# Kernel tuning notes

Hardware: AMD Instinct MI355X
Metric: run time of the kernel (lower is better)

The kernel has to match this reference:

```python
import jax, jax.numpy as jnp
import numpy as np

MARGIN = 0.2  # TripletMarginLoss margin and TripletMarginMiner margin


def setup_inputs() -> dict:
    key = jax.random.key(0)
    k1, k2 = jax.random.split(key)
    embeddings = jax.random.normal(k1, (384, 256), dtype=jnp.float32)
    labels = jax.random.randint(k2, (384,), 0, 32)
    return {"embeddings": embeddings, "labels": labels}


def _pairwise_l2(e):
    # Euclidean distance matrix with sqrt-safe gradient at zero.
    sq = jnp.sum(e * e, axis=1)
    d2 = jnp.maximum(sq[:, None] + sq[None, :] - 2.0 * (e @ e.T), 0.0)
    pos = d2 > 0.0
    return jnp.sqrt(jnp.where(pos, d2, 1.0)) * pos


def reference(embeddings, labels):
    # pytorch-metric-learning LpDistance defaults: normalize_embeddings=True, p=2
    e = embeddings / jnp.maximum(
        jnp.linalg.norm(embeddings, axis=1, keepdims=True), 1e-12
    )
    D = _pairwise_l2(e)  # [B, B]
    n = D.shape[0]

    same = labels[:, None] == labels[None, :]
    eye = jnp.eye(n, dtype=bool)
    pos_mask = same & ~eye   # valid (anchor, positive) pairs
    neg_mask = ~same         # valid (anchor, negative) pairs

    ap = D[:, :, None]       # dist(anchor, positive), broadcast over negative
    an = D[:, None, :]       # dist(anchor, negative), broadcast over positive
    tm = an - ap             # miner's triplet_margin (is_inverted=False)

    valid = pos_mask[:, :, None] & neg_mask[:, None, :]     # [B, B, B]
    # semihard miner: 0 < an - ap <= margin
    semihard = valid & (tm > 0.0) & (tm <= MARGIN)

    # TripletMarginLoss per-triplet loss: relu(ap - an + margin) = relu(margin - tm)
    losses = jnp.where(semihard, jnp.maximum(MARGIN - tm, 0.0), 0.0)

    # AvgNonZeroReducer: mean over strictly-positive losses (0 if none)
    nz = jnp.sum(losses > 0.0)
    total = jnp.sum(losses)
    return jnp.where(nz > 0, total / jnp.maximum(nz, 1).astype(total.dtype), 0.0)
```

## Files before the change

### kernel.cpp

```cpp
#include <hip/hip_runtime.h>

#define N        384
#define DIM      256
#define MARGIN_F 0.2f
#define NANCH    2
#define NBLK     (N / NANCH)


__global__ __launch_bounds__(DIM) void normalize_kernel(
    const float* __restrict__ emb, float* __restrict__ eT,
    float* __restrict__ sq, float* __restrict__ invn,
    float* __restrict__ accum_sum, unsigned int* __restrict__ accum_cnt,
    unsigned int* __restrict__ done_cnt)
{
    const int row = blockIdx.x;
    const int tid = threadIdx.x;

    float v = emb[row * DIM + tid];
    float s = v * v;
    #pragma unroll
    for (int off = 32; off > 0; off >>= 1) s += __shfl_down(s, off, 64);
    __shared__ float wsum[4];
    const int wave = tid >> 6, lane = tid & 63;
    if (lane == 0) wsum[wave] = s;
    __syncthreads();
    if (tid == 0) wsum[0] = wsum[0] + wsum[1] + wsum[2] + wsum[3];
    __syncthreads();
    const float tot = wsum[0];

    const float inv = 1.0f / fmaxf(sqrtf(tot), 1e-12f);
    eT[tid * N + row] = v * inv;

    if (tid == 0) {
        sq[row]   = tot * inv * inv;
        invn[row] = inv;
        if (row == 0) { accum_sum[0] = 0.0f; accum_cnt[0] = 0u; done_cnt[0] = 0u; }
    }
}

__global__ __launch_bounds__(N) void fused_kernel(
    const float* __restrict__ emb, const float* __restrict__ eT,
    const float* __restrict__ sq, const float* __restrict__ invn,
    const int* __restrict__ labels,
    float* __restrict__ accum_sum, unsigned int* __restrict__ accum_cnt,
    unsigned int* __restrict__ done_cnt, float* __restrict__ out)
{
    const int i0  = blockIdx.x * NANCH;
    const int tid = threadIdx.x;

    __shared__ float ei[NANCH][DIM];
    __shared__ float Drow[NANCH][N];
    __shared__ int   lab[N];
    __shared__ int   posList[NANCH][N];
    __shared__ int   posCnt[NANCH];
    __shared__ float sredS[N / 64];
    __shared__ unsigned int sredC[N / 64];

    for (int t = tid; t < NANCH * DIM; t += N) {
        const int a = t >> 8, k = t & (DIM - 1);
        ei[a][k] = emb[(i0 + a) * DIM + k] * invn[i0 + a];
    }
    lab[tid] = labels[tid];
    if (tid < NANCH) posCnt[tid] = 0;
    __syncthreads();

    float acc0 = 0.0f, acc1 = 0.0f;
    const float* __restrict__ col = eT + tid;
    #pragma unroll 8
    for (int k = 0; k < DIM; ++k) {
        const float ek = col[k * N];
        acc0 += ei[0][k] * ek;
        acc1 += ei[1][k] * ek;
    }
    const float sqj = sq[tid];
    {
        const float d2 = fmaxf(sq[i0] + sqj - 2.0f * acc0, 0.0f);
        Drow[0][tid] = (d2 > 0.0f) ? sqrtf(d2) : 0.0f;
    }
    {
        const float d2 = fmaxf(sq[i0 + 1] + sqj - 2.0f * acc1, 0.0f);
        Drow[1][tid] = (d2 > 0.0f) ? sqrtf(d2) : 0.0f;
    }
    __syncthreads();

    const int lj = lab[tid];
    #pragma unroll
    for (int a = 0; a < NANCH; ++a) {
        const int ia = i0 + a;
        if (lj == lab[ia] && tid != ia)
            posList[a][atomicAdd(&posCnt[a], 1)] = tid;
    }
    __syncthreads();

    float        lsum = 0.0f;
    unsigned int lcnt = 0u;
    #pragma unroll
    for (int a = 0; a < NANCH; ++a) {
        const int   li = lab[i0 + a];
        const float dk = Drow[a][tid];
        if (lj != li) {
            const int np = posCnt[a];
            for (int p = 0; p < np; ++p) {
                const float tm = dk - Drow[a][posList[a][p]];
                if (tm > 0.0f && tm <= MARGIN_F) {
                    const float l = MARGIN_F - tm;
                    lsum += l;
                    if (l > 0.0f) lcnt++;
                }
            }
        }
    }

    #pragma unroll
    for (int off = 32; off > 0; off >>= 1) {
        lsum += __shfl_down(lsum, off, 64);
        lcnt += __shfl_down(lcnt, off, 64);
    }
    const int wave = tid >> 6, lane = tid & 63;
    if (lane == 0) { sredS[wave] = lsum; sredC[wave] = lcnt; }
    __syncthreads();

    if (tid == 0) {
        float        S = 0.0f;
        unsigned int C = 0u;
        #pragma unroll
        for (int w = 0; w < N / 64; ++w) { S += sredS[w]; C += sredC[w]; }
        if (S != 0.0f || C != 0u) {
            atomicAdd(accum_sum, S);
            atomicAdd(accum_cnt, C);
        }
        __threadfence();
        const unsigned int prev = atomicAdd(done_cnt, 1);
        if (prev == NBLK - 1) {
            const float        Sall = atomicAdd(accum_sum, 0.0f);
            const unsigned int Call = atomicAdd(accum_cnt, 0u);
            out[0] = (Call > 0u) ? (Sall / (float)Call) : 0.0f;
        }
    }
}

extern "C" void kernel_launch(void* const* d_in, const int* in_sizes, int n_in,
                              void* d_out, int out_size, void* d_ws, size_t ws_size,
                              hipStream_t stream) {
    const float* emb    = (const float*)d_in[0];
    const int*   labels = (const int*)d_in[1];
    float*       out    = (float*)d_out;

    float* ws   = (float*)d_ws;
    float* eT   = ws;
    float* sq   = eT + (size_t)DIM * N;
    float* invn = sq + N;
    float* accum_sum = invn + N;
    unsigned int* accum_cnt = (unsigned int*)(accum_sum + 1);
    unsigned int* done_cnt  = accum_cnt + 1;

    normalize_kernel<<<N, DIM, 0, stream>>>(emb, eT, sq, invn,
                                            accum_sum, accum_cnt, done_cnt);
    fused_kernel<<<NBLK, N, 0, stream>>>(emb, eT, sq, invn, labels,
                                         accum_sum, accum_cnt, done_cnt, out);
}
```

Measured before the change: 78.53 us.

## Fuse normalization into main kernel and read row-major embeddings with float4

Removes the separate normalize kernel and the transposed eT workspace. Each block now recomputes every row norm itself, and the dot products read raw embedding rows as float4, with the column's inverse norm applied afterwards. Accumulators are zeroed with a memset. Each of the 192 blocks redundantly reads the full embedding matrix to compute norms, and each thread's row-wise float4 reads are strided across threads instead of coalesced. The positive list is capped at 64 entries, which is unsafe if a class has more than 64 members.

```diff
diff --git a/kernel.cpp b/kernel.cpp
--- a/kernel.cpp
+++ b/kernel.cpp
@@ -2,83 +2,74 @@
 
 #define N        384
 #define DIM      256
+#define D4       (DIM / 4)
 #define MARGIN_F 0.2f
 #define NANCH    2
 #define NBLK     (N / NANCH)
+#define NTHR     384
+#define NWAVE    (NTHR / 64)
+#define MAXPOS   64
 
 
-__global__ __launch_bounds__(DIM) void normalize_kernel(
-    const float* __restrict__ emb, float* __restrict__ eT,
-    float* __restrict__ sq, float* __restrict__ invn,
-    float* __restrict__ accum_sum, unsigned int* __restrict__ accum_cnt,
-    unsigned int* __restrict__ done_cnt)
-{
-    const int row = blockIdx.x;
-    const int tid = threadIdx.x;
-
-    float v = emb[row * DIM + tid];
-    float s = v * v;
-    #pragma unroll
-    for (int off = 32; off > 0; off >>= 1) s += __shfl_down(s, off, 64);
-    __shared__ float wsum[4];
-    const int wave = tid >> 6, lane = tid & 63;
-    if (lane == 0) wsum[wave] = s;
-    __syncthreads();
-    if (tid == 0) wsum[0] = wsum[0] + wsum[1] + wsum[2] + wsum[3];
-    __syncthreads();
-    const float tot = wsum[0];
-
-    const float inv = 1.0f / fmaxf(sqrtf(tot), 1e-12f);
-    eT[tid * N + row] = v * inv;
-
-    if (tid == 0) {
-        sq[row]   = tot * inv * inv;
-        invn[row] = inv;
-        if (row == 0) { accum_sum[0] = 0.0f; accum_cnt[0] = 0u; done_cnt[0] = 0u; }
-    }
-}
-
-__global__ __launch_bounds__(N) void fused_kernel(
-    const float* __restrict__ emb, const float* __restrict__ eT,
-    const float* __restrict__ sq, const float* __restrict__ invn,
-    const int* __restrict__ labels,
+__global__ __launch_bounds__(NTHR) void fused_all(
+    const float* __restrict__ emb, const int* __restrict__ labels,
     float* __restrict__ accum_sum, unsigned int* __restrict__ accum_cnt,
     unsigned int* __restrict__ done_cnt, float* __restrict__ out)
 {
-    const int i0  = blockIdx.x * NANCH;
-    const int tid = threadIdx.x;
+    const int i0   = blockIdx.x * NANCH;
+    const int tid  = threadIdx.x;
+    const int wave = tid >> 6, lane = tid & 63;
 
+    __shared__ float invn[N];
+    __shared__ float sqn[N];
     __shared__ float ei[NANCH][DIM];
     __shared__ float Drow[NANCH][N];
     __shared__ int   lab[N];
-    __shared__ int   posList[NANCH][N];
+    __shared__ int   posList[NANCH][MAXPOS];
     __shared__ int   posCnt[NANCH];
-    __shared__ float sredS[N / 64];
-    __shared__ unsigned int sredC[N / 64];
+    __shared__ float        sredS[NWAVE];
+    __shared__ unsigned int sredC[NWAVE];
 
-    for (int t = tid; t < NANCH * DIM; t += N) {
+    const float4* emb4 = (const float4*)emb;
+    for (int r = wave; r < N; r += NWAVE) {
+        const float4 v = emb4[r * D4 + lane];
+        float s = v.x*v.x + v.y*v.y + v.z*v.z + v.w*v.w;
+        #pragma unroll
+        for (int off = 32; off > 0; off >>= 1) s += __shfl_down(s, off, 64);
+        if (lane == 0) {
+            const float inv = 1.0f / fmaxf(sqrtf(s), 1e-12f);
+            invn[r] = inv;
+            sqn[r]  = s * inv * inv;
+        }
+    }
+    if (tid < NANCH) posCnt[tid] = 0;
+    lab[tid] = labels[tid];
+    __syncthreads();
+
+    for (int t = tid; t < NANCH * DIM; t += NTHR) {
         const int a = t >> 8, k = t & (DIM - 1);
         ei[a][k] = emb[(i0 + a) * DIM + k] * invn[i0 + a];
     }
-    lab[tid] = labels[tid];
-    if (tid < NANCH) posCnt[tid] = 0;
     __syncthreads();
 
+    const float4* __restrict__ rowj = emb4 + (size_t)tid * D4;
+    const float4* __restrict__ e0   = (const float4*)ei[0];
+    const float4* __restrict__ e1   = (const float4*)ei[1];
     float acc0 = 0.0f, acc1 = 0.0f;
-    const float* __restrict__ col = eT + tid;
     #pragma unroll 8
-    for (int k = 0; k < DIM; ++k) {
-        const float ek = col[k * N];
-        acc0 += ei[0][k] * ek;
-        acc1 += ei[1][k] * ek;
+    for (int k = 0; k < D4; ++k) {
+        const float4 v  = rowj[k];
+        const float4 a0 = e0[k];
+        const float4 a1 = e1[k];
+        acc0 += v.x*a0.x + v.y*a0.y + v.z*a0.z + v.w*a0.w;
+        acc1 += v.x*a1.x + v.y*a1.y + v.z*a1.z + v.w*a1.w;
     }
-    const float sqj = sq[tid];
+    const float invj = invn[tid];
+    const float sqj  = sqn[tid];
     {
-        const float d2 = fmaxf(sq[i0] + sqj - 2.0f * acc0, 0.0f);
+        float d2 = fmaxf(sqn[i0]     + sqj - 2.0f * acc0 * invj, 0.0f);
         Drow[0][tid] = (d2 > 0.0f) ? sqrtf(d2) : 0.0f;
-    }
-    {
-        const float d2 = fmaxf(sq[i0 + 1] + sqj - 2.0f * acc1, 0.0f);
+        d2       = fmaxf(sqn[i0 + 1] + sqj - 2.0f * acc1 * invj, 0.0f);
         Drow[1][tid] = (d2 > 0.0f) ? sqrtf(d2) : 0.0f;
     }
     __syncthreads();
@@ -116,7 +107,6 @@
         lsum += __shfl_down(lsum, off, 64);
         lcnt += __shfl_down(lcnt, off, 64);
     }
-    const int wave = tid >> 6, lane = tid & 63;
     if (lane == 0) { sredS[wave] = lsum; sredC[wave] = lcnt; }
     __syncthreads();
 
@@ -124,7 +114,7 @@
         float        S = 0.0f;
         unsigned int C = 0u;
         #pragma unroll
-        for (int w = 0; w < N / 64; ++w) { S += sredS[w]; C += sredC[w]; }
+        for (int w = 0; w < NWAVE; ++w) { S += sredS[w]; C += sredC[w]; }
         if (S != 0.0f || C != 0u) {
             atomicAdd(accum_sum, S);
             atomicAdd(accum_cnt, C);
@@ -146,16 +136,11 @@
     const int*   labels = (const int*)d_in[1];
     float*       out    = (float*)d_out;
 
-    float* ws   = (float*)d_ws;
-    float* eT   = ws;
-    float* sq   = eT + (size_t)DIM * N;
-    float* invn = sq + N;
-    float* accum_sum = invn + N;
-    unsigned int* accum_cnt = (unsigned int*)(accum_sum + 1);
-    unsigned int* done_cnt  = accum_cnt + 1;
+    float*        accum_sum = (float*)d_ws;
+    unsigned int* accum_cnt = (unsigned int*)accum_sum + 1;
+    unsigned int* done_cnt  = (unsigned int*)accum_sum + 2;
 
-    normalize_kernel<<<N, DIM, 0, stream>>>(emb, eT, sq, invn,
-                                            accum_sum, accum_cnt, done_cnt);
-    fused_kernel<<<NBLK, N, 0, stream>>>(emb, eT, sq, invn, labels,
+    hipMemsetAsync(d_ws, 0, 12, stream);
+    fused_all<<<NBLK, NTHR, 0, stream>>>(emb, labels,
                                          accum_sum, accum_cnt, done_cnt, out);
 }
```

Result: slower. 110.6 us (+40.8%).
